# Kernel optimization log

Measured on AMD Instinct MI355X. Metric: run time of the kernel, lower is better.

## Reference

```python
import jax, jax.numpy as jnp
import numpy as np

B, T, N, D, H, C = 32, 64, 22, 512, 8, 128
DEPTH = D // H


def setup_inputs() -> dict:
    key = jax.random.key(0)
    ks = jax.random.split(key, 10)
    s = 0.02
    return {
        "x": jax.random.normal(ks[0], (B, T, N, D), jnp.float32),
        "context": jax.random.normal(ks[1], (B, C, D), jnp.float32),
        "Wq": jax.random.normal(ks[2], (N, D, D), jnp.float32) * s,  # per-joint Q proj
        "bq": jax.random.normal(ks[3], (N, D), jnp.float32) * s,
        "Wk": jax.random.normal(ks[4], (D, D), jnp.float32) * s,
        "bk": jax.random.normal(ks[5], (D,), jnp.float32) * s,
        "Wv": jax.random.normal(ks[6], (D, D), jnp.float32) * s,
        "bv": jax.random.normal(ks[7], (D,), jnp.float32) * s,
        "Wout": jax.random.normal(ks[8], (D, D), jnp.float32) * s,
        "bout": jax.random.normal(ks[9], (D,), jnp.float32) * s,
    }


def reference(x, context, Wq, bq, Wk, bk, Wv, bv, Wout, bout):
    b, t, n, d = x.shape
    c = context.shape[1]
    h, dh = H, DEPTH
    # Per-joint Q projection fused into one batched GEMM: [B,T,N,D] x [N,D,D] -> [B,T,N,D]
    q = jnp.einsum('btnd,ndf->btnf', x, Wq) + bq  # bq broadcasts over (B,T)
    # Shared K/V computed ONCE (original recomputes per joint; math identical)
    k = context @ Wk + bk  # [B,C,D]
    v = context @ Wv + bv  # [B,C,D]
    # Split heads
    qh = q.reshape(b, t, n, h, dh)
    kh = k.reshape(b, c, h, dh)
    vh = v.reshape(b, c, h, dh)
    scale = 1.0 / float(np.sqrt(dh))
    # Attention logits per joint: [B,N,H,T,C]
    logits = jnp.einsum('btnhd,bchd->bnhtc', qh, kh) * scale
    attn = jax.nn.softmax(logits, axis=-1)
    # Attend shared V, merge heads: [B,T,N,D]
    o = jnp.einsum('bnhtc,bchd->btnhd', attn, vh).reshape(b, t, n, d)
    # Shared output projection
    return o @ Wout + bout
```

## Files before the change

### kernel.cpp

```cpp
#include <hip/hip_runtime.h>
#include <hip/hip_bf16.h>

#define NB 32
#define NT 64
#define NJ 22
#define ND 512
#define NH 8
#define NC 128
#define NDH 64
#define NR 1408

typedef __attribute__((ext_vector_type(8))) short s16x8;
typedef __attribute__((ext_vector_type(4))) float fx4;

static __device__ __forceinline__ unsigned short f2bf(float f) {
    unsigned u = __builtin_bit_cast(unsigned, f);
    u += 0x7fffu + ((u >> 16) & 1u);
    return (unsigned short)(u >> 16);
}

static __device__ __forceinline__ fx4 mfma16(s16x8 a, s16x8 b, fx4 c) {
    return __builtin_amdgcn_mfma_f32_16x16x32_bf16(a, b, c, 0, 0, 0);
}

static __device__ __forceinline__ void gload16(const void* g, void* l) {
    __builtin_amdgcn_global_load_lds(
        (const __attribute__((address_space(1))) void*)g,
        (__attribute__((address_space(3))) void*)l,
        16, 0, 0);
}

__global__ __launch_bounds__(256) void convx_k(const float* __restrict__ src,
                                               unsigned short* __restrict__ dst)
{
    const long i = ((long)blockIdx.x * 256 + threadIdx.x) * 8;
    const float4 a = *reinterpret_cast<const float4*>(src + i);
    const float4 b = *reinterpret_cast<const float4*>(src + i + 4);
    unsigned short t[8];
    t[0]=f2bf(a.x); t[1]=f2bf(a.y); t[2]=f2bf(a.z); t[3]=f2bf(a.w);
    t[4]=f2bf(b.x); t[5]=f2bf(b.y); t[6]=f2bf(b.z); t[7]=f2bf(b.w);
    *reinterpret_cast<s16x8*>(dst + i) = *reinterpret_cast<s16x8*>(t);
}

__global__ __launch_bounds__(256) void twconv_k(const float* __restrict__ W,
                                                unsigned short* __restrict__ Wt,
                                                long zsrc, long zdst)
{
    __shared__ float T[64][65];
    const int tid = threadIdx.x;
    W  += blockIdx.z * zsrc + (long)blockIdx.x * 64 * 512 + blockIdx.y * 64;
    Wt += blockIdx.z * zdst + (long)blockIdx.y * 64 * 512 + blockIdx.x * 64;
    const int r = tid >> 2, c0 = (tid & 3) * 16;
    #pragma unroll
    for (int i = 0; i < 4; ++i) {
        const float4 p = *reinterpret_cast<const float4*>(W + (long)r * 512 + c0 + i*4);
        T[r][c0 + i*4 + 0] = p.x; T[r][c0 + i*4 + 1] = p.y;
        T[r][c0 + i*4 + 2] = p.z; T[r][c0 + i*4 + 3] = p.w;
    }
    __syncthreads();
    unsigned short o[16];
    #pragma unroll
    for (int i = 0; i < 16; ++i) o[i] = f2bf(T[c0 + i][r]);
    *reinterpret_cast<s16x8*>(Wt + (long)r * 512 + c0)     = *reinterpret_cast<s16x8*>(o);
    *reinterpret_cast<s16x8*>(Wt + (long)r * 512 + c0 + 8) = *reinterpret_cast<s16x8*>(o + 8);
}

template <typename TC, int MODE>
__global__ __launch_bounds__(256) void gemm128_k(
    const unsigned short* __restrict__ A, long lda,
    const unsigned short* __restrict__ Bt,
    const float* __restrict__ bias,
    TC* __restrict__ C, long ldc,
    long jsA, long jsW, long jsB, long jsC)
{
    __shared__ unsigned short As[128][64];
    __shared__ unsigned short Bs[128][64];

    const int tid = threadIdx.x;
    const int w = tid >> 6, lane = tid & 63;
    const long j = blockIdx.z;

    A    += (long)blockIdx.x * 128 * lda + j * jsA;
    Bt   += j * jsW + (long)blockIdx.y * 128 * 512;
    bias += j * jsB + blockIdx.y * 128;
    if constexpr (MODE == 0)
        C += (long)blockIdx.x * 128 * ldc + j * jsC + blockIdx.y * 128;

    const int srow = lane >> 3;
    const int scol = (lane & 7) * 8;
    const unsigned short* Ag = A  + (long)(w*8 + srow) * lda + scol;
    const unsigned short* Bg = Bt + (long)(w*8 + srow) * 512 + scol;
    char* Al = (char*)As + w * 1024;
    char* Bl = (char*)Bs + w * 1024;

    const int lr = lane & 15, lk = lane >> 4;
    const int wm = w >> 1, wn = w & 1;

    fx4 acc[4][4] = {};

    for (int kt = 0; kt < 512; kt += 64) {
        #pragma unroll
        for (int it = 0; it < 4; ++it)
            gload16(Ag + (long)it * 32 * lda + kt, Al + it * 4096);
        #pragma unroll
        for (int it = 0; it < 4; ++it)
            gload16(Bg + (long)it * 32 * 512 + kt, Bl + it * 4096);
        __syncthreads();
        #pragma unroll
        for (int ks = 0; ks < 2; ++ks) {
            s16x8 a[4], b[4];
            #pragma unroll
            for (int m = 0; m < 4; ++m)
                a[m] = *reinterpret_cast<const s16x8*>(&As[wm*64 + m*16 + lr][ks*32 + lk*8]);
            #pragma unroll
            for (int n = 0; n < 4; ++n)
                b[n] = *reinterpret_cast<const s16x8*>(&Bs[wn*64 + n*16 + lr][ks*32 + lk*8]);
            #pragma unroll
            for (int m = 0; m < 4; ++m)
                #pragma unroll
                for (int n = 0; n < 4; ++n)
                    acc[m][n] = mfma16(a[m], b[n], acc[m][n]);
        }
        __syncthreads();
    }

    #pragma unroll
    for (int n = 0; n < 4; ++n) {
        const int col = wn*64 + n*16 + lr;
        const float bv = bias[col];
        #pragma unroll
        for (int m = 0; m < 4; ++m) {
            #pragma unroll
            for (int r = 0; r < 4; ++r) {
                const int row = wm*64 + m*16 + lk*4 + r;
                const float val = acc[m][n][r] + bv;
                if constexpr (MODE == 0) {
                    if constexpr (sizeof(TC) == 2)
                        reinterpret_cast<unsigned short*>(C)[(long)row*ldc + col] = f2bf(val);
                    else
                        reinterpret_cast<float*>(C)[(long)row*ldc + col] = val;
                } else {
                    const int grow = blockIdx.x*128 + row;
                    const int gcol = blockIdx.y*128 + col;
                    const int b = grow >> 7, c = grow & 127;
                    const int hh = gcol >> 6, dh = gcol & 63;
                    unsigned short* Cp = reinterpret_cast<unsigned short*>(C);
                    if constexpr (MODE == 1) {
                        const int dhs = (dh & 7) | ((((dh >> 3) ^ (c & 7)) & 7) << 3);
                        Cp[(((long)b*8 + hh)*128 + c)*64 + dhs] = f2bf(val);
                    } else {
                        const int cs = (c & 7) | ((((c >> 3) ^ (dh & 7)) & 15) << 3);
                        Cp[(((long)b*8 + hh)*64 + dh)*128 + cs] = f2bf(val);
                    }
                }
            }
        }
    }
}

__global__ __launch_bounds__(256) void attn2_k(
    const unsigned short* __restrict__ q,
    const unsigned short* __restrict__ kt,
    const unsigned short* __restrict__ vt,
    unsigned short* __restrict__ o)
{
    __shared__ unsigned short Ps[128*136];
    __shared__ unsigned short Ks[128*64];
    __shared__ unsigned short Vs[64*128];

    const int tid = threadIdx.x;
    const int w = tid >> 6, lane = tid & 63;
    const int lr = lane & 15, lk = lane >> 4;
    const int r0 = blockIdx.x * 128;
    const int h = blockIdx.y;
    const int b = blockIdx.z;

    const unsigned short* qg = q + ((long)b*NR + r0 + w*32 + (lane>>3))*512
                                 + h*64 + (lane & 7)*8;
    const unsigned short* kg = kt + ((long)(b*8+h))*8192 + (w*4)*512 + lane*8;
    const unsigned short* vg = vt + ((long)(b*8+h))*8192 + (w*4)*512 + lane*8;

    #pragma unroll
    for (int it = 0; it < 4; ++it) {
        gload16(qg + (long)it*8*512, (char*)Ps + (w*32 + it*8)*128);
        gload16(kg + it*512, (char*)Ks + (w*4 + it)*1024);
        gload16(vg + it*512, (char*)Vs + (w*4 + it)*1024);
    }
    __syncthreads();

    s16x8 aq[2][2];
    #pragma unroll
    for (int m = 0; m < 2; ++m)
        #pragma unroll
        for (int kk = 0; kk < 2; ++kk)
            aq[m][kk] = *reinterpret_cast<const s16x8*>(
                &Ps[(w*32 + m*16 + lr)*64 + kk*32 + lk*8]);
    __syncthreads();

    fx4 s[2][8] = {};
    #pragma unroll
    for (int kk = 0; kk < 2; ++kk) {
        #pragma unroll
        for (int f = 0; f < 8; ++f) {
            const int c = f*16 + lr;
            const int chunk = (kk*4 + lk) ^ (c & 7);
            s16x8 bk = *reinterpret_cast<const s16x8*>(&Ks[c*64 + chunk*8]);
            s[0][f] = mfma16(aq[0][kk], bk, s[0][f]);
            s[1][f] = mfma16(aq[1][kk], bk, s[1][f]);
        }
    }

    const float SC = 0.125f * 1.44269504088896340736f;
    #pragma unroll
    for (int m = 0; m < 2; ++m) {
        #pragma unroll
        for (int r = 0; r < 4; ++r) {
            float mx = -3.0e38f;
            #pragma unroll
            for (int f = 0; f < 8; ++f) mx = fmaxf(mx, s[m][f][r]);
            #pragma unroll
            for (int off = 1; off < 16; off <<= 1) mx = fmaxf(mx, __shfl_xor(mx, off));
            float p[8]; float sum = 0.f;
            #pragma unroll
            for (int f = 0; f < 8; ++f) {
                p[f] = exp2f((s[m][f][r] - mx) * SC);
                sum += p[f];
            }
            #pragma unroll
            for (int off = 1; off < 16; off <<= 1) sum += __shfl_xor(sum, off);
            const float inv = 1.0f / sum;
            const int row = w*32 + m*16 + lk*4 + r;
            #pragma unroll
            for (int f = 0; f < 8; ++f)
                Ps[row*136 + f*16 + lr] = f2bf(p[f] * inv);
        }
    }

    fx4 oacc[2][4] = {};
    #pragma unroll
    for (int kt4 = 0; kt4 < 4; ++kt4) {
        s16x8 ap[2];
        #pragma unroll
        for (int m = 0; m < 2; ++m)
            ap[m] = *reinterpret_cast<const s16x8*>(
                &Ps[(w*32 + m*16 + lr)*136 + kt4*32 + lk*8]);
        #pragma unroll
        for (int bn = 0; bn < 4; ++bn) {
            const int dh = bn*16 + lr;
            const int chunk = (kt4*4 + lk) ^ (dh & 7);
            s16x8 bv = *reinterpret_cast<const s16x8*>(&Vs[dh*128 + chunk*8]);
            oacc[0][bn] = mfma16(ap[0], bv, oacc[0][bn]);
            oacc[1][bn] = mfma16(ap[1], bv, oacc[1][bn]);
        }
    }

    unsigned short* ob = o + ((long)b*NR + r0)*512 + h*64;
    #pragma unroll
    for (int m = 0; m < 2; ++m)
        #pragma unroll
        for (int bn = 0; bn < 4; ++bn)
            #pragma unroll
            for (int r = 0; r < 4; ++r) {
                const int row = w*32 + m*16 + lk*4 + r;
                ob[(long)row*512 + bn*16 + lr] = f2bf(oacc[m][bn][r]);
            }
}

extern "C" void kernel_launch(void* const* d_in, const int* in_sizes, int n_in,
                              void* d_out, int out_size, void* d_ws, size_t ws_size,
                              hipStream_t stream)
{
    const float* x    = (const float*)d_in[0];
    const float* ctx  = (const float*)d_in[1];
    const float* Wq   = (const float*)d_in[2];
    const float* bq   = (const float*)d_in[3];
    const float* Wk   = (const float*)d_in[4];
    const float* bk   = (const float*)d_in[5];
    const float* Wv   = (const float*)d_in[6];
    const float* bv   = (const float*)d_in[7];
    const float* Wout = (const float*)d_in[8];
    const float* bout = (const float*)d_in[9];
    float* out = (float*)d_out;

    const size_t NX  = (size_t)45056 * 512;
    const size_t NKV = (size_t)4096 * 512;
    const size_t NW  = (size_t)512 * 512;

    unsigned short* xbf   = (unsigned short*)d_ws;
    unsigned short* qbf   = xbf   + NX;
    unsigned short* cbf   = qbf   + NX;
    unsigned short* ktp   = cbf   + NKV;
    unsigned short* vtp   = ktp   + NKV;
    unsigned short* WqT   = vtp   + NKV;
    unsigned short* WkT   = WqT   + 22 * NW;
    unsigned short* WvT   = WkT   + NW;
    unsigned short* WoutT = WvT   + NW;
    unsigned short* obf   = xbf;

    convx_k<<<dim3(NX / 2048), 256, 0, stream>>>(x, xbf);
    convx_k<<<dim3(NKV / 2048), 256, 0, stream>>>(ctx, cbf);
    twconv_k<<<dim3(8, 8, 22), 256, 0, stream>>>(Wq,   WqT,   (long)NW, (long)NW);
    twconv_k<<<dim3(8, 8, 1),  256, 0, stream>>>(Wk,   WkT,   0, 0);
    twconv_k<<<dim3(8, 8, 1),  256, 0, stream>>>(Wv,   WvT,   0, 0);
    twconv_k<<<dim3(8, 8, 1),  256, 0, stream>>>(Wout, WoutT, 0, 0);

    gemm128_k<unsigned short, 0><<<dim3(16, 4, NJ), 256, 0, stream>>>(
        xbf, (long)NJ*ND, WqT, bq, qbf, (long)NJ*ND,
        (long)ND, (long)NW, (long)ND, (long)ND);

    gemm128_k<unsigned short, 1><<<dim3(32, 4, 1), 256, 0, stream>>>(
        cbf, ND, WkT, bk, ktp, ND, 0, 0, 0, 0);
    gemm128_k<unsigned short, 2><<<dim3(32, 4, 1), 256, 0, stream>>>(
        cbf, ND, WvT, bv, vtp, ND, 0, 0, 0, 0);

    attn2_k<<<dim3(NR/128, NH, NB), 256, 0, stream>>>(qbf, ktp, vtp, obf);

    gemm128_k<float, 0><<<dim3(45056/128, 4, 1), 256, 0, stream>>>(
        obf, ND, WoutT, bout, out, ND, 0, 0, 0, 0);
}
```

Before: 213.6 us.

## Double-buffer GEMM LDS tiles, XOR-swizzle operand layouts, and remap workgroup order

The GEMM kernel now keeps two LDS buffers, so the next K-tile's global-to-LDS loads are issued before the current tile is computed, with one barrier per step instead of two. The producer kernels (input conversion, weight transpose, attention output store) now write bf16 data with an XOR chunk swizzle keyed on the row. This lets the GEMM read LDS fragments without bank conflicts, since global_load_lds copies the data straight through. Workgroup IDs are also remapped so that neighbouring blocks share operand tiles for better cache reuse. The cost is double the LDS per block, which may reduce occupancy, plus a strict coupling of swizzle conventions across several kernels.

```diff
diff --git a/kernel.cpp b/kernel.cpp
--- a/kernel.cpp
+++ b/kernel.cpp
@@ -30,16 +30,22 @@
         16, 0, 0);
 }
 
-__global__ __launch_bounds__(256) void convx_k(const float* __restrict__ src,
-                                               unsigned short* __restrict__ dst)
+template <int DIV>
+__global__ __launch_bounds__(256) void convswz_k(const float* __restrict__ src,
+                                                 unsigned short* __restrict__ dst)
 {
     const long i = ((long)blockIdx.x * 256 + threadIdx.x) * 8;
+    const unsigned row = (unsigned)(i >> 9);
+    const int  key = (int)((row / (unsigned)DIV) & 7u);
+    const int  c   = (int)((i >> 3) & 7);
+    const int  cs  = c ^ key;
+    const long j   = (i & ~63L) | ((long)cs << 3);
     const float4 a = *reinterpret_cast<const float4*>(src + i);
     const float4 b = *reinterpret_cast<const float4*>(src + i + 4);
     unsigned short t[8];
     t[0]=f2bf(a.x); t[1]=f2bf(a.y); t[2]=f2bf(a.z); t[3]=f2bf(a.w);
     t[4]=f2bf(b.x); t[5]=f2bf(b.y); t[6]=f2bf(b.z); t[7]=f2bf(b.w);
-    *reinterpret_cast<s16x8*>(dst + i) = *reinterpret_cast<s16x8*>(t);
+    *reinterpret_cast<s16x8*>(dst + j) = *reinterpret_cast<s16x8*>(t);
 }
 
 __global__ __launch_bounds__(256) void twconv_k(const float* __restrict__ W,
@@ -61,8 +67,9 @@
     unsigned short o[16];
     #pragma unroll
     for (int i = 0; i < 16; ++i) o[i] = f2bf(T[c0 + i][r]);
-    *reinterpret_cast<s16x8*>(Wt + (long)r * 512 + c0)     = *reinterpret_cast<s16x8*>(o);
-    *reinterpret_cast<s16x8*>(Wt + (long)r * 512 + c0 + 8) = *reinterpret_cast<s16x8*>(o + 8);
+    const int ch0 = ((c0 >> 3) ^ (r & 7));
+    *reinterpret_cast<s16x8*>(Wt + (long)r * 512 + ch0*8)       = *reinterpret_cast<s16x8*>(o);
+    *reinterpret_cast<s16x8*>(Wt + (long)r * 512 + (ch0^1)*8)   = *reinterpret_cast<s16x8*>(o + 8);
 }
 
 template <typename TC, int MODE>
@@ -73,56 +80,75 @@
     TC* __restrict__ C, long ldc,
     long jsA, long jsW, long jsB, long jsC)
 {
-    __shared__ unsigned short As[128][64];
-    __shared__ unsigned short Bs[128][64];
+    __shared__ unsigned short As[2][128*64];
+    __shared__ unsigned short Bs[2][128*64];
 
     const int tid = threadIdx.x;
     const int w = tid >> 6, lane = tid & 63;
     const long j = blockIdx.z;
 
-    A    += (long)blockIdx.x * 128 * lda + j * jsA;
-    Bt   += j * jsW + (long)blockIdx.y * 128 * 512;
-    bias += j * jsB + blockIdx.y * 128;
+    const int nx = gridDim.x;
+    const int nwg = nx * gridDim.y;
+    int lin = blockIdx.y * nx + blockIdx.x;
+    lin = (lin & 7) * (nwg >> 3) + (lin >> 3);
+    const int bx = lin % nx, by = lin / nx;
+
+    A    += (long)bx * 128 * lda + j * jsA;
+    Bt   += j * jsW + (long)by * 128 * 512;
+    bias += j * jsB + by * 128;
     if constexpr (MODE == 0)
-        C += (long)blockIdx.x * 128 * ldc + j * jsC + blockIdx.y * 128;
+        C += (long)bx * 128 * ldc + j * jsC + by * 128;
 
     const int srow = lane >> 3;
     const int scol = (lane & 7) * 8;
     const unsigned short* Ag = A  + (long)(w*8 + srow) * lda + scol;
     const unsigned short* Bg = Bt + (long)(w*8 + srow) * 512 + scol;
-    char* Al = (char*)As + w * 1024;
-    char* Bl = (char*)Bs + w * 1024;
 
     const int lr = lane & 15, lk = lane >> 4;
     const int wm = w >> 1, wn = w & 1;
 
     fx4 acc[4][4] = {};
 
-    for (int kt = 0; kt < 512; kt += 64) {
+    auto STAGE = [&](int buf, int kt) {
+        char* Al = (char*)&As[buf][0] + w * 1024;
+        char* Bl = (char*)&Bs[buf][0] + w * 1024;
         #pragma unroll
         for (int it = 0; it < 4; ++it)
             gload16(Ag + (long)it * 32 * lda + kt, Al + it * 4096);
         #pragma unroll
         for (int it = 0; it < 4; ++it)
             gload16(Bg + (long)it * 32 * 512 + kt, Bl + it * 4096);
-        __syncthreads();
+    };
+
+    auto COMPUTE = [&](int buf) {
         #pragma unroll
         for (int ks = 0; ks < 2; ++ks) {
+            const int cha = (ks*4 + lk) ^ (lr & 7);
             s16x8 a[4], b[4];
             #pragma unroll
             for (int m = 0; m < 4; ++m)
-                a[m] = *reinterpret_cast<const s16x8*>(&As[wm*64 + m*16 + lr][ks*32 + lk*8]);
+                a[m] = *reinterpret_cast<const s16x8*>(&As[buf][(wm*64 + m*16 + lr)*64 + cha*8]);
             #pragma unroll
             for (int n = 0; n < 4; ++n)
-                b[n] = *reinterpret_cast<const s16x8*>(&Bs[wn*64 + n*16 + lr][ks*32 + lk*8]);
+                b[n] = *reinterpret_cast<const s16x8*>(&Bs[buf][(wn*64 + n*16 + lr)*64 + cha*8]);
             #pragma unroll
             for (int m = 0; m < 4; ++m)
                 #pragma unroll
                 for (int n = 0; n < 4; ++n)
                     acc[m][n] = mfma16(a[m], b[n], acc[m][n]);
         }
+    };
+
+    STAGE(0, 0);
+    __syncthreads();
+    #pragma unroll
+    for (int t = 0; t < 7; ++t) {
+        const int cur = t & 1;
+        STAGE(cur ^ 1, (t + 1) * 64);
+        COMPUTE(cur);
         __syncthreads();
     }
+    COMPUTE(1);
 
     #pragma unroll
     for (int n = 0; n < 4; ++n) {
@@ -140,8 +166,8 @@
                     else
                         reinterpret_cast<float*>(C)[(long)row*ldc + col] = val;
                 } else {
-                    const int grow = blockIdx.x*128 + row;
-                    const int gcol = blockIdx.y*128 + col;
+                    const int grow = bx*128 + row;
+                    const int gcol = by*128 + col;
                     const int b = grow >> 7, c = grow & 127;
                     const int hh = gcol >> 6, dh = gcol & 63;
                     unsigned short* Cp = reinterpret_cast<unsigned short*>(C);
@@ -262,7 +288,9 @@
             #pragma unroll
             for (int r = 0; r < 4; ++r) {
                 const int row = w*32 + m*16 + lk*4 + r;
-                ob[(long)row*512 + bn*16 + lr] = f2bf(oacc[m][bn][r]);
+                const int colg = bn*16 + lr;
+                const int ch = ((colg >> 3) ^ (row & 7));
+                ob[(long)row*512 + ch*8 + (lr & 7)] = f2bf(oacc[m][bn][r]);
             }
 }
 
@@ -297,8 +325,8 @@
     unsigned short* WoutT = WvT   + NW;
     unsigned short* obf   = xbf;
 
-    convx_k<<<dim3(NX / 2048), 256, 0, stream>>>(x, xbf);
-    convx_k<<<dim3(NKV / 2048), 256, 0, stream>>>(ctx, cbf);
+    convswz_k<NJ><<<dim3(NX / 2048), 256, 0, stream>>>(x, xbf);
+    convswz_k<1><<<dim3(NKV / 2048), 256, 0, stream>>>(ctx, cbf);
     twconv_k<<<dim3(8, 8, 22), 256, 0, stream>>>(Wq,   WqT,   (long)NW, (long)NW);
     twconv_k<<<dim3(8, 8, 1),  256, 0, stream>>>(Wk,   WkT,   0, 0);
     twconv_k<<<dim3(8, 8, 1),  256, 0, stream>>>(Wv,   WvT,   0, 0);
```

Result: faster. 207.8 us (-2.7%).
